# Kernel optimization log

Hardware: AMD Instinct MI355X
Metric: run time of the kernel (lower is better)

The kernel has to match this reference:

```python
import jax, jax.numpy as jnp
import numpy as np


def setup_inputs() -> dict:
    key = jax.random.key(0)
    k1, k2 = jax.random.split(key)
    B, H, W, C = 32, 32, 32, 256
    N_EMBED = 1024
    z = jax.random.normal(k1, (B, H, W, C), dtype=jnp.float32)
    emb_weights = jax.random.normal(k2, (N_EMBED, C), dtype=jnp.float32)
    return {"z": z, "emb_weights": emb_weights}


def reference(z, emb_weights):
    # z: (B,H,W,C) -> flatten to (N, C)
    B = z.shape[0]
    C = z.shape[-1]
    z_flat = z.reshape(-1, C)  # (N, C)
    # Squared euclidean distance via ||z||^2 + ||e||^2 - 2 z.e^T
    distance = (
        jnp.sum(z_flat ** 2, axis=1, keepdims=True)          # (N, 1)
        + jnp.sum(emb_weights ** 2, axis=1)                   # (n_embed,)
        - 2.0 * jnp.dot(z_flat, emb_weights.T)                # (N, n_embed)
    )
    min_encoding_indices = jnp.argmin(distance, axis=1)       # (N,)
    z_q = emb_weights[min_encoding_indices].reshape(z.shape)  # (B,H,W,C)
    min_encoding_indices = min_encoding_indices.reshape(B, -1)
    return z_q, min_encoding_indices
```

## Files before the change

kernel.cpp:

```cpp
#include <hip/hip_runtime.h>

#define C_DIM 256
#define NCODE 1024
#define MARGIN1 0.35f
#define MARGIN2 0.02f

typedef __bf16 bf16x8 __attribute__((ext_vector_type(8)));
typedef float f32x4 __attribute__((ext_vector_type(4)));

#define WS_ENORM  0
#define WS_META   4096
#define WS_RLIST  8192
#define WS_RLIST2 139264
#define WS_BP     270336
#define WS_PB     1318912
#define WS_PBI    2367488

#define BP_LO_OFF 262144

#define GLOAD_LDS16(g, s)                                                            \
  __builtin_amdgcn_global_load_lds(                                                  \
      (const __attribute__((address_space(1))) unsigned int*)(g),                    \
      (__attribute__((address_space(3))) unsigned int*)(s), 16, 0, 0)

__device__ __forceinline__ unsigned short bf16rne(float x) {
    unsigned u = __float_as_uint(x);
    return (unsigned short)((u + 0x7FFFu + ((u >> 16) & 1u)) >> 16);
}
__device__ __forceinline__ void bf16split(float x, unsigned short& h, unsigned short& l) {
    unsigned u  = __float_as_uint(x);
    unsigned rh = (u + 0x7FFFu + ((u >> 16) & 1u)) & 0xFFFF0000u;
    float    lf = x - __uint_as_float(rh);
    h = (unsigned short)(rh >> 16);
    l = bf16rne(lf);
}

__global__ __launch_bounds__(256) void prep_kernel(const float* __restrict__ emb,
                                                   unsigned short* __restrict__ bp,
                                                   float* __restrict__ enorm,
                                                   unsigned* __restrict__ meta) {
    int tid = blockIdx.x * 256 + threadIdx.x;
    if (tid < 2) meta[tid] = 0u;
    int j   = tid >> 5;
    int u   = tid & 31;
    int kc  = u >> 2, lg = u & 3;
    const float* src = emb + (size_t)j * C_DIM + kc * 32 + lg * 8;
    float4 v0 = *reinterpret_cast<const float4*>(src);
    float4 v1 = *reinterpret_cast<const float4*>(src + 4);
    float vs[8] = {v0.x, v0.y, v0.z, v0.w, v1.x, v1.y, v1.z, v1.w};
    unsigned short h[8], l[8];
    float s = 0.f;
    #pragma unroll
    for (int k = 0; k < 8; ++k) {
        bf16split(vs[k], h[k], l[k]);
        s = fmaf(vs[k], vs[k], s);
    }
    #pragma unroll
    for (int off = 1; off < 32; off <<= 1) s += __shfl_xor(s, off, 64);
    if (u == 0) enorm[j] = s;

    int chunk = j >> 5, nf = (j >> 4) & 1, lr = j & 15;
    int lane  = lg * 16 + lr;
    size_t base = (size_t)chunk * 8192 + (size_t)(nf * 8 + kc) * 512 + lane * 8;
    uint4 hp, lp;
    hp.x = (unsigned)h[0] | ((unsigned)h[1] << 16);
    hp.y = (unsigned)h[2] | ((unsigned)h[3] << 16);
    hp.z = (unsigned)h[4] | ((unsigned)h[5] << 16);
    hp.w = (unsigned)h[6] | ((unsigned)h[7] << 16);
    lp.x = (unsigned)l[0] | ((unsigned)l[1] << 16);
    lp.y = (unsigned)l[2] | ((unsigned)l[3] << 16);
    lp.z = (unsigned)l[4] | ((unsigned)l[5] << 16);
    lp.w = (unsigned)l[6] | ((unsigned)l[7] << 16);
    *reinterpret_cast<uint4*>(bp + base)             = hp;
    *reinterpret_cast<uint4*>(bp + BP_LO_OFF + base) = lp;
}

__global__ __launch_bounds__(256, 4) void vq_stage1_kernel(
    const float* __restrict__ z, const unsigned short* __restrict__ bp,
    const float* __restrict__ enorm, float2* __restrict__ pb,
    unsigned* __restrict__ pbi) {
    __shared__ unsigned short Bds[2][8192];
    __shared__ float en_s[256];

    const int t = threadIdx.x;
    const int w = t >> 6, lane = t & 63;
    const int lr = lane & 15, lg = lane >> 4;
    const int nq = blockIdx.x & 3;
    const long r0 = (long)(blockIdx.x >> 2) * 128 + w * 32;
    const unsigned short* bsrc = bp + (size_t)(nq * 8) * 8192 + lane * 8;

    en_s[t] = enorm[nq * 256 + t];

    bf16x8 ah[2][8];
    #pragma unroll
    for (int m = 0; m < 2; ++m) {
        const float* zr = z + (r0 + m * 16 + lr) * C_DIM + lg * 8;
        #pragma unroll
        for (int kc = 0; kc < 8; ++kc) {
            float4 v0 = *reinterpret_cast<const float4*>(zr + kc * 32);
            float4 v1 = *reinterpret_cast<const float4*>(zr + kc * 32 + 4);
            float vs[8] = {v0.x, v0.y, v0.z, v0.w, v1.x, v1.y, v1.z, v1.w};
            unsigned hp[4];
            #pragma unroll
            for (int p = 0; p < 4; ++p)
                hp[p] = (unsigned)bf16rne(vs[2 * p]) |
                        ((unsigned)bf16rne(vs[2 * p + 1]) << 16);
            ah[m][kc] = __builtin_bit_cast(bf16x8, *reinterpret_cast<uint4*>(hp));
        }
    }
    __syncthreads();

#define STG1(c, sl) {                                                   \
    unsigned short* db = &Bds[sl][0];                                   \
    const unsigned short* gs = bsrc + (size_t)(c) * 8192;               \
    _Pragma("unroll") for (int rd = 0; rd < 4; ++rd) {                  \
        int s_ = rd * 4 + w;                                            \
        GLOAD_LDS16(gs + s_ * 512, db + s_ * 512); } }

    STG1(0, 0);

    float b1[2][4], b2[2][4]; unsigned i1[2][4];
    #pragma unroll
    for (int m = 0; m < 2; ++m)
        #pragma unroll
        for (int r = 0; r < 4; ++r) { b1[m][r] = 3.4e38f; b2[m][r] = 3.4e38f; i1[m][r] = 0; }

    #pragma unroll 1
    for (int c = 0; c < 8; ++c) {
        asm volatile("s_waitcnt vmcnt(0)" ::: "memory");
        __builtin_amdgcn_s_barrier();
        if (c < 7) STG1(c + 1, (c + 1) & 1);

        f32x4 a00 = {0.f,0.f,0.f,0.f}, a01 = {0.f,0.f,0.f,0.f};
        f32x4 a10 = {0.f,0.f,0.f,0.f}, a11 = {0.f,0.f,0.f,0.f};
        const unsigned short* bb = &Bds[c & 1][lane * 8];
        __builtin_amdgcn_s_setprio(1);
        #pragma unroll
        for (int kc = 0; kc < 8; ++kc) {
            bf16x8 bh0 = *reinterpret_cast<const bf16x8*>(bb + kc * 512);
            bf16x8 bh1 = *reinterpret_cast<const bf16x8*>(bb + (8 + kc) * 512);
            a00 = __builtin_amdgcn_mfma_f32_16x16x32_bf16(ah[0][kc], bh0, a00, 0, 0, 0);
            a10 = __builtin_amdgcn_mfma_f32_16x16x32_bf16(ah[1][kc], bh0, a10, 0, 0, 0);
            a01 = __builtin_amdgcn_mfma_f32_16x16x32_bf16(ah[0][kc], bh1, a01, 0, 0, 0);
            a11 = __builtin_amdgcn_mfma_f32_16x16x32_bf16(ah[1][kc], bh1, a11, 0, 0, 0);
        }
        __builtin_amdgcn_s_setprio(0);

        #pragma unroll
        for (int nf = 0; nf < 2; ++nf) {
            const int cl = c * 32 + nf * 16 + lr;
            const float en = en_s[cl];
            const unsigned code = (unsigned)(nq * 256 + cl);
            #pragma unroll
            for (int r = 0; r < 4; ++r) {
                float d0 = fmaf(-2.f, (nf ? a01[r] : a00[r]), en);
                if (d0 < b1[0][r]) { b2[0][r] = b1[0][r]; b1[0][r] = d0; i1[0][r] = code; }
                else if (d0 < b2[0][r]) { b2[0][r] = d0; }
                float d1 = fmaf(-2.f, (nf ? a11[r] : a10[r]), en);
                if (d1 < b1[1][r]) { b2[1][r] = b1[1][r]; b1[1][r] = d1; i1[1][r] = code; }
                else if (d1 < b2[1][r]) { b2[1][r] = d1; }
            }
        }
    }
#undef STG1

    #pragma unroll
    for (int m = 0; m < 2; ++m)
        #pragma unroll
        for (int r = 0; r < 4; ++r) {
            float v1 = b1[m][r], v2 = b2[m][r]; unsigned j1 = i1[m][r];
            #pragma unroll
            for (int off = 8; off; off >>= 1) {
                float    ov1 = __shfl_xor(v1, off, 64);
                float    ov2 = __shfl_xor(v2, off, 64);
                unsigned oj1 = (unsigned)__shfl_xor((int)j1, off, 64);
                if (ov1 < v1 || (ov1 == v1 && oj1 < j1)) {
                    v2 = fminf(v1, ov2); v1 = ov1; j1 = oj1;
                } else {
                    v2 = fminf(v2, ov1);
                }
            }
            if (lr == 0) {
                long row = r0 + m * 16 + lg * 4 + r;
                pb [row * 4 + nq] = make_float2(v1, v2);
                pbi[row * 4 + nq] = j1;
            }
        }
}

__global__ __launch_bounds__(256) void finalize_gather_kernel(
    const float* __restrict__ emb, const float2* __restrict__ pb,
    const unsigned* __restrict__ pbi, float* __restrict__ zq,
    float* __restrict__ idx_out, unsigned* __restrict__ meta,
    unsigned* __restrict__ rlist, int n4) {
    const int lane = threadIdx.x & 63;
    for (long r4 = blockIdx.x; r4 < n4; r4 += gridDim.x) {
        const long row = r4 * 4 + (threadIdx.x >> 6);
        float B1 = 3.4e38f, B2 = 3.4e38f; unsigned I1 = 0;
        #pragma unroll
        for (int s = 0; s < 4; ++s) {
            float2   p = pb [row * 4 + s];
            unsigned j = pbi[row * 4 + s];
            if (p.x < B1) { B2 = fminf(B1, p.y); B1 = p.x; I1 = j; }
            else          { B2 = fminf(B2, p.x); }
        }
        if (lane == 0) {
            idx_out[row] = (float)I1;
            if (B2 - B1 <= MARGIN1) rlist[atomicAdd(meta, 1u)] = (unsigned)row;
        }
        float4 v = reinterpret_cast<const float4*>(emb)[(size_t)I1 * 64 + lane];
        reinterpret_cast<float4*>(zq)[row * 64 + lane] = v;
    }
}

__global__ __launch_bounds__(256) void vq_stage2_kernel(
    const float* __restrict__ z, const unsigned short* __restrict__ bp,
    const float* __restrict__ enorm, const float* __restrict__ emb,
    const unsigned* __restrict__ meta, const unsigned* __restrict__ rlist,
    float* __restrict__ zq, float* __restrict__ idx_out,
    unsigned* __restrict__ meta2, unsigned* __restrict__ rlist2) {
    __shared__ float en_s[NCODE];
    __shared__ float m1s[16][4], m2s[16][4];
    __shared__ unsigned mis[16][4];
    __shared__ unsigned codes_s[16];
    const int t = threadIdx.x, q = t >> 6, lane = t & 63;
    const int lr = lane & 15, lg = lane >> 4;
    en_s[t] = enorm[t]; en_s[t + 256] = enorm[t + 256];
    en_s[t + 512] = enorm[t + 512]; en_s[t + 768] = enorm[t + 768];
    __syncthreads();
    const unsigned cnt = meta[0];
    const unsigned ngroups = (cnt + 15) >> 4;

    for (unsigned g = blockIdx.x; g < ngroups; g += gridDim.x) {
        const unsigned base = g * 16;
        unsigned slot = base + (unsigned)lr;
        unsigned row = rlist[slot < cnt ? slot : 0];

        bf16x8 ah[8], al[8];
        const float* zr = z + (size_t)row * C_DIM + lg * 8;
        #pragma unroll
        for (int kc = 0; kc < 8; ++kc) {
            float4 v0 = *reinterpret_cast<const float4*>(zr + kc * 32);
            float4 v1 = *reinterpret_cast<const float4*>(zr + kc * 32 + 4);
            float vs[8] = {v0.x, v0.y, v0.z, v0.w, v1.x, v1.y, v1.z, v1.w};
            unsigned short hv[8], lv[8];
            #pragma unroll
            for (int jj = 0; jj < 8; ++jj) bf16split(vs[jj], hv[jj], lv[jj]);
            unsigned hp[4] = {
                (unsigned)hv[0] | ((unsigned)hv[1] << 16), (unsigned)hv[2] | ((unsigned)hv[3] << 16),
                (unsigned)hv[4] | ((unsigned)hv[5] << 16), (unsigned)hv[6] | ((unsigned)hv[7] << 16)};
            unsigned lp[4] = {
                (unsigned)lv[0] | ((unsigned)lv[1] << 16), (unsigned)lv[2] | ((unsigned)lv[3] << 16),
                (unsigned)lv[4] | ((unsigned)lv[5] << 16), (unsigned)lv[6] | ((unsigned)lv[7] << 16)};
            ah[kc] = __builtin_bit_cast(bf16x8, *reinterpret_cast<uint4*>(hp));
            al[kc] = __builtin_bit_cast(bf16x8, *reinterpret_cast<uint4*>(lp));
        }

        float b1[4], b2[4]; unsigned i1[4];
        #pragma unroll
        for (int r = 0; r < 4; ++r) { b1[r] = 3.4e38f; b2[r] = 3.4e38f; i1[r] = 0; }

        #pragma unroll 1
        for (int cc = 0; cc < 8; ++cc) {
            const int c = q * 8 + cc;
            f32x4 hh0 = {0.f,0.f,0.f,0.f}, hh1 = {0.f,0.f,0.f,0.f};
            f32x4 hl0 = {0.f,0.f,0.f,0.f}, hl1 = {0.f,0.f,0.f,0.f};
            f32x4 lh0 = {0.f,0.f,0.f,0.f}, lh1 = {0.f,0.f,0.f,0.f};
            const unsigned short* cb = bp + (size_t)c * 8192 + lane * 8;
            #pragma unroll
            for (int kc = 0; kc < 8; ++kc) {
                bf16x8 bh0 = *reinterpret_cast<const bf16x8*>(cb + kc * 512);
                bf16x8 bh1 = *reinterpret_cast<const bf16x8*>(cb + (8 + kc) * 512);
                bf16x8 bl0 = *reinterpret_cast<const bf16x8*>(cb + BP_LO_OFF + kc * 512);
                bf16x8 bl1 = *reinterpret_cast<const bf16x8*>(cb + BP_LO_OFF + (8 + kc) * 512);
                hh0 = __builtin_amdgcn_mfma_f32_16x16x32_bf16(ah[kc], bh0, hh0, 0, 0, 0);
                hh1 = __builtin_amdgcn_mfma_f32_16x16x32_bf16(ah[kc], bh1, hh1, 0, 0, 0);
                lh0 = __builtin_amdgcn_mfma_f32_16x16x32_bf16(al[kc], bh0, lh0, 0, 0, 0);
                lh1 = __builtin_amdgcn_mfma_f32_16x16x32_bf16(al[kc], bh1, lh1, 0, 0, 0);
                hl0 = __builtin_amdgcn_mfma_f32_16x16x32_bf16(ah[kc], bl0, hl0, 0, 0, 0);
                hl1 = __builtin_amdgcn_mfma_f32_16x16x32_bf16(ah[kc], bl1, hl1, 0, 0, 0);
            }
            #pragma unroll
            for (int nf = 0; nf < 2; ++nf) {
                const unsigned code = (unsigned)(c * 32 + nf * 16 + lr);
                const float en = en_s[code];
                #pragma unroll
                for (int r = 0; r < 4; ++r) {
                    float s3 = nf ? (hh1[r] + hl1[r] + lh1[r]) : (hh0[r] + hl0[r] + lh0[r]);
                    float d = fmaf(-2.f, s3, en);
                    if (d < b1[r]) { b2[r] = b1[r]; b1[r] = d; i1[r] = code; }
                    else if (d < b2[r]) { b2[r] = d; }
                }
            }
        }

        #pragma unroll
        for (int r = 0; r < 4; ++r) {
            float v1 = b1[r], v2 = b2[r]; unsigned j1 = i1[r];
            #pragma unroll
            for (int off = 8; off; off >>= 1) {
                float    ov1 = __shfl_xor(v1, off, 64);
                float    ov2 = __shfl_xor(v2, off, 64);
                unsigned oj1 = (unsigned)__shfl_xor((int)j1, off, 64);
                if (ov1 < v1 || (ov1 == v1 && oj1 < j1)) {
                    v2 = fminf(v1, ov2); v1 = ov1; j1 = oj1;
                } else {
                    v2 = fminf(v2, ov1);
                }
            }
            if (lr == 0) {
                int rg = lg * 4 + r;
                m1s[rg][q] = v1; m2s[rg][q] = v2; mis[rg][q] = j1;
            }
        }
        __syncthreads();
        if (t < 16) {
            float B1 = 3.4e38f, B2 = 3.4e38f; unsigned I1 = 0;
            #pragma unroll
            for (int s = 0; s < 4; ++s) {
                float v1 = m1s[t][s], v2 = m2s[t][s]; unsigned j = mis[t][s];
                if (v1 < B1) { B2 = fminf(B1, v2); B1 = v1; I1 = j; }
                else         { B2 = fminf(B2, v1); }
            }
            unsigned sl = base + (unsigned)t;
            codes_s[t] = I1;
            if (sl < cnt) {
                unsigned rrow = rlist[sl];
                idx_out[rrow] = (float)I1;
                if (B2 - B1 <= MARGIN2) rlist2[atomicAdd(meta2, 1u)] = rrow;
            }
        }
        __syncthreads();
        {
            int rr = t >> 4, seg = t & 15;
            unsigned sl = base + (unsigned)rr;
            if (sl < cnt) {
                unsigned rrow = rlist[sl];
                unsigned code = codes_s[rr];
                const float4* ep = reinterpret_cast<const float4*>(emb) + (size_t)code * 64 + seg * 4;
                float4*       op = reinterpret_cast<float4*>(zq) + (size_t)rrow * 64 + seg * 4;
                op[0] = ep[0]; op[1] = ep[1]; op[2] = ep[2]; op[3] = ep[3];
            }
        }
        __syncthreads();
    }
}

__global__ __launch_bounds__(256) void rescue_kernel(
    const float* __restrict__ z, const float* __restrict__ emb,
    const float* __restrict__ enorm, const unsigned* __restrict__ meta2,
    const unsigned* __restrict__ rlist2, float* __restrict__ zq,
    float* __restrict__ idx_out) {
    __shared__ float zrow[C_DIM];
    __shared__ float rd[256];
    __shared__ unsigned rix[256];
    const unsigned cnt = meta2[0];
    for (unsigned li = blockIdx.x; li < cnt; li += gridDim.x) {
        unsigned row = rlist2[li];
        __syncthreads();
        if (threadIdx.x < 64) {
            float4 v = reinterpret_cast<const float4*>(z)[(size_t)row * 64 + threadIdx.x];
            reinterpret_cast<float4*>(zrow)[threadIdx.x] = v;
        }
        __syncthreads();
        const int c = threadIdx.x;
        float a0 = 0.f, a1 = 0.f, a2 = 0.f, a3 = 0.f;
        const float4* zp = reinterpret_cast<const float4*>(zrow);
        const float4* e0 = reinterpret_cast<const float4*>(emb + (size_t)(c)       * C_DIM);
        const float4* e1 = reinterpret_cast<const float4*>(emb + (size_t)(c + 256) * C_DIM);
        const float4* e2 = reinterpret_cast<const float4*>(emb + (size_t)(c + 512) * C_DIM);
        const float4* e3 = reinterpret_cast<const float4*>(emb + (size_t)(c + 768) * C_DIM);
        #pragma unroll 8
        for (int k = 0; k < 64; ++k) {
            float4 z4 = zp[k];
            float4 f0 = e0[k], f1 = e1[k], f2 = e2[k], f3 = e3[k];
            a0 = fmaf(z4.x, f0.x, a0); a0 = fmaf(z4.y, f0.y, a0);
            a0 = fmaf(z4.z, f0.z, a0); a0 = fmaf(z4.w, f0.w, a0);
            a1 = fmaf(z4.x, f1.x, a1); a1 = fmaf(z4.y, f1.y, a1);
            a1 = fmaf(z4.z, f1.z, a1); a1 = fmaf(z4.w, f1.w, a1);
            a2 = fmaf(z4.x, f2.x, a2); a2 = fmaf(z4.y, f2.y, a2);
            a2 = fmaf(z4.z, f2.z, a2); a2 = fmaf(z4.w, f2.w, a2);
            a3 = fmaf(z4.x, f3.x, a3); a3 = fmaf(z4.y, f3.y, a3);
            a3 = fmaf(z4.z, f3.z, a3); a3 = fmaf(z4.w, f3.w, a3);
        }
        float d0 = fmaf(-2.f, a0, enorm[c]);
        float d1 = fmaf(-2.f, a1, enorm[c + 256]);
        float d2 = fmaf(-2.f, a2, enorm[c + 512]);
        float d3 = fmaf(-2.f, a3, enorm[c + 768]);
        float bd = d0; unsigned bi = (unsigned)c;
        if (d1 < bd) { bd = d1; bi = (unsigned)(c + 256); }
        if (d2 < bd) { bd = d2; bi = (unsigned)(c + 512); }
        if (d3 < bd) { bd = d3; bi = (unsigned)(c + 768); }
        rd[threadIdx.x] = bd; rix[threadIdx.x] = bi;
        __syncthreads();
        for (int s = 128; s; s >>= 1) {
            if (threadIdx.x < (unsigned)s) {
                float od = rd[threadIdx.x + s]; unsigned oi = rix[threadIdx.x + s];
                if (od < rd[threadIdx.x] ||
                    (od == rd[threadIdx.x] && oi < rix[threadIdx.x])) {
                    rd[threadIdx.x] = od; rix[threadIdx.x] = oi;
                }
            }
            __syncthreads();
        }
        unsigned code = rix[0];
        if (threadIdx.x < 64) {
            float4 v = reinterpret_cast<const float4*>(emb)[(size_t)code * 64 + threadIdx.x];
            reinterpret_cast<float4*>(zq)[(size_t)row * 64 + threadIdx.x] = v;
        }
        if (threadIdx.x == 0) idx_out[row] = (float)code;
    }
}

extern "C" void kernel_launch(void* const* d_in, const int* in_sizes, int n_in,
                              void* d_out, int out_size, void* d_ws, size_t ws_size,
                              hipStream_t stream) {
    const float* z   = (const float*)d_in[0];
    const float* emb = (const float*)d_in[1];
    const int n = in_sizes[0] / C_DIM;

    float* zq      = (float*)d_out;
    float* idx_out = zq + (size_t)n * C_DIM;

    char* ws = (char*)d_ws;
    float*          enorm  = (float*)(ws + WS_ENORM);
    unsigned*       meta   = (unsigned*)(ws + WS_META);
    unsigned*       rlist  = (unsigned*)(ws + WS_RLIST);
    unsigned*       rlist2 = (unsigned*)(ws + WS_RLIST2);
    unsigned short* bp     = (unsigned short*)(ws + WS_BP);
    float2*         pb     = (float2*)(ws + WS_PB);
    unsigned*       pbi    = (unsigned*)(ws + WS_PBI);

    prep_kernel<<<128, 256, 0, stream>>>(emb, bp, enorm, meta);
    vq_stage1_kernel<<<(n / 128) * 4, 256, 0, stream>>>(z, bp, enorm, pb, pbi);
    finalize_gather_kernel<<<2048, 256, 0, stream>>>(emb, pb, pbi, zq, idx_out,
                                                     meta, rlist, n / 4);
    vq_stage2_kernel<<<256, 256, 0, stream>>>(z, bp, enorm, emb, meta, rlist,
                                              zq, idx_out, meta + 1, rlist2);
    rescue_kernel<<<256, 256, 0, stream>>>(z, emb, enorm, meta + 1, rlist2,
                                           zq, idx_out);
}
```

Measured before the change: 135.5 us.

## Fuse finalize, stage-2 refinement and rescue into one per-block kernel

Replaces the finalize/gather, stage-2 refinement and rescue kernels with a single kernel in which each block handles 32 rows. Ambiguous rows are tracked in shared-memory lists rather than global atomic lists. This removes two kernel launches, the global atomic counters and the meta zeroing. In exchange, refinement and rescue work is no longer spread across blocks, so a block with many flagged rows serialises that work. The rescue loop runs fp32 matmuls inside a 256-thread block per row, which can create load imbalance.

```diff
diff --git a/kernel.cpp b/kernel.cpp
--- a/kernel.cpp
+++ b/kernel.cpp
@@ -9,13 +9,9 @@
 typedef float f32x4 __attribute__((ext_vector_type(4)));
 
 #define WS_ENORM  0
-#define WS_META   4096
-#define WS_RLIST  8192
-#define WS_RLIST2 139264
 #define WS_BP     270336
 #define WS_PB     1318912
 #define WS_PBI    2367488
-
 #define BP_LO_OFF 262144
 
 #define GLOAD_LDS16(g, s)                                                            \
@@ -37,10 +33,8 @@
 
 __global__ __launch_bounds__(256) void prep_kernel(const float* __restrict__ emb,
                                                    unsigned short* __restrict__ bp,
-                                                   float* __restrict__ enorm,
-                                                   unsigned* __restrict__ meta) {
+                                                   float* __restrict__ enorm) {
     int tid = blockIdx.x * 256 + threadIdx.x;
-    if (tid < 2) meta[tid] = 0u;
     int j   = tid >> 5;
     int u   = tid & 31;
     int kc  = u >> 2, lg = u & 3;
@@ -188,14 +182,35 @@
         }
 }
 
-__global__ __launch_bounds__(256) void finalize_gather_kernel(
-    const float* __restrict__ emb, const float2* __restrict__ pb,
-    const unsigned* __restrict__ pbi, float* __restrict__ zq,
-    float* __restrict__ idx_out, unsigned* __restrict__ meta,
-    unsigned* __restrict__ rlist, int n4) {
-    const int lane = threadIdx.x & 63;
-    for (long r4 = blockIdx.x; r4 < n4; r4 += gridDim.x) {
-        const long row = r4 * 4 + (threadIdx.x >> 6);
+__global__ __launch_bounds__(256) void finalize_all_kernel(
+    const float* __restrict__ z, const unsigned short* __restrict__ bp,
+    const float* __restrict__ enorm, const float* __restrict__ emb,
+    const float2* __restrict__ pb, const unsigned* __restrict__ pbi,
+    float* __restrict__ zq, float* __restrict__ idx_out) {
+    __shared__ float en_s[NCODE];
+    __shared__ float m1s[16][4], m2s[16][4];
+    __shared__ unsigned mis[16][4];
+    __shared__ unsigned codes_b[16];
+    __shared__ unsigned codes_a[32];
+    __shared__ unsigned flag_r[32];
+    __shared__ unsigned flag_n;
+    __shared__ unsigned resc_r[16];
+    __shared__ unsigned resc_n;
+    __shared__ float zrow[C_DIM];
+    __shared__ float rd[256];
+    __shared__ unsigned rix[256];
+
+    const int t = threadIdx.x, q = t >> 6, lane = t & 63;
+    const int lr = lane & 15, lg = lane >> 4;
+    const long r0 = (long)blockIdx.x * 32;
+
+    en_s[t] = enorm[t]; en_s[t + 256] = enorm[t + 256];
+    en_s[t + 512] = enorm[t + 512]; en_s[t + 768] = enorm[t + 768];
+    if (t == 0) flag_n = 0u;
+    __syncthreads();
+
+    if (t < 32) {
+        long row = r0 + t;
         float B1 = 3.4e38f, B2 = 3.4e38f; unsigned I1 = 0;
         #pragma unroll
         for (int s = 0; s < 4; ++s) {
@@ -204,37 +219,26 @@
             if (p.x < B1) { B2 = fminf(B1, p.y); B1 = p.x; I1 = j; }
             else          { B2 = fminf(B2, p.x); }
         }
-        if (lane == 0) {
-            idx_out[row] = (float)I1;
-            if (B2 - B1 <= MARGIN1) rlist[atomicAdd(meta, 1u)] = (unsigned)row;
-        }
-        float4 v = reinterpret_cast<const float4*>(emb)[(size_t)I1 * 64 + lane];
-        reinterpret_cast<float4*>(zq)[row * 64 + lane] = v;
-    }
-}
-
-__global__ __launch_bounds__(256) void vq_stage2_kernel(
-    const float* __restrict__ z, const unsigned short* __restrict__ bp,
-    const float* __restrict__ enorm, const float* __restrict__ emb,
-    const unsigned* __restrict__ meta, const unsigned* __restrict__ rlist,
-    float* __restrict__ zq, float* __restrict__ idx_out,
-    unsigned* __restrict__ meta2, unsigned* __restrict__ rlist2) {
-    __shared__ float en_s[NCODE];
-    __shared__ float m1s[16][4], m2s[16][4];
-    __shared__ unsigned mis[16][4];
-    __shared__ unsigned codes_s[16];
-    const int t = threadIdx.x, q = t >> 6, lane = t & 63;
-    const int lr = lane & 15, lg = lane >> 4;
-    en_s[t] = enorm[t]; en_s[t + 256] = enorm[t + 256];
-    en_s[t + 512] = enorm[t + 512]; en_s[t + 768] = enorm[t + 768];
+        idx_out[row] = (float)I1;
+        codes_a[t]   = I1;
+        if (B2 - B1 <= MARGIN1) flag_r[atomicAdd(&flag_n, 1u)] = (unsigned)row;
+    }
     __syncthreads();
-    const unsigned cnt = meta[0];
-    const unsigned ngroups = (cnt + 15) >> 4;
-
-    for (unsigned g = blockIdx.x; g < ngroups; g += gridDim.x) {
-        const unsigned base = g * 16;
+    {
+        int rr = t >> 3, seg = t & 7;
+        unsigned code = codes_a[rr];
+        const float4* ep = reinterpret_cast<const float4*>(emb) + (size_t)code * 64 + seg * 8;
+        float4*       op = reinterpret_cast<float4*>(zq) + ((size_t)(r0 + rr)) * 64 + seg * 8;
+        #pragma unroll
+        for (int j = 0; j < 8; ++j) op[j] = ep[j];
+    }
+    __syncthreads();
+
+    const unsigned nflag = flag_n;
+    for (unsigned base = 0; base < nflag; base += 16) {
         unsigned slot = base + (unsigned)lr;
-        unsigned row = rlist[slot < cnt ? slot : 0];
+        unsigned row = flag_r[slot < nflag ? slot : 0];
+        if (t == 0) resc_n = 0u;
 
         bf16x8 ah[8], al[8];
         const float* zr = z + (size_t)row * C_DIM + lg * 8;
@@ -323,92 +327,83 @@
                 else         { B2 = fminf(B2, v1); }
             }
             unsigned sl = base + (unsigned)t;
-            codes_s[t] = I1;
-            if (sl < cnt) {
-                unsigned rrow = rlist[sl];
+            codes_b[t] = I1;
+            if (sl < nflag) {
+                unsigned rrow = flag_r[sl];
                 idx_out[rrow] = (float)I1;
-                if (B2 - B1 <= MARGIN2) rlist2[atomicAdd(meta2, 1u)] = rrow;
+                if (B2 - B1 <= MARGIN2) resc_r[atomicAdd(&resc_n, 1u)] = rrow;
             }
         }
         __syncthreads();
         {
             int rr = t >> 4, seg = t & 15;
             unsigned sl = base + (unsigned)rr;
-            if (sl < cnt) {
-                unsigned rrow = rlist[sl];
-                unsigned code = codes_s[rr];
+            if (sl < nflag) {
+                unsigned rrow = flag_r[sl];
+                unsigned code = codes_b[rr];
                 const float4* ep = reinterpret_cast<const float4*>(emb) + (size_t)code * 64 + seg * 4;
                 float4*       op = reinterpret_cast<float4*>(zq) + (size_t)rrow * 64 + seg * 4;
                 op[0] = ep[0]; op[1] = ep[1]; op[2] = ep[2]; op[3] = ep[3];
             }
         }
         __syncthreads();
-    }
-}
-
-__global__ __launch_bounds__(256) void rescue_kernel(
-    const float* __restrict__ z, const float* __restrict__ emb,
-    const float* __restrict__ enorm, const unsigned* __restrict__ meta2,
-    const unsigned* __restrict__ rlist2, float* __restrict__ zq,
-    float* __restrict__ idx_out) {
-    __shared__ float zrow[C_DIM];
-    __shared__ float rd[256];
-    __shared__ unsigned rix[256];
-    const unsigned cnt = meta2[0];
-    for (unsigned li = blockIdx.x; li < cnt; li += gridDim.x) {
-        unsigned row = rlist2[li];
+
+        const unsigned nresc = resc_n;
+        for (unsigned ri = 0; ri < nresc; ++ri) {
+            unsigned rrow = resc_r[ri];
+            if (t < 64) {
+                float4 v = reinterpret_cast<const float4*>(z)[(size_t)rrow * 64 + t];
+                reinterpret_cast<float4*>(zrow)[t] = v;
+            }
+            __syncthreads();
+            const int c = t;
+            float a0 = 0.f, a1 = 0.f, a2 = 0.f, a3 = 0.f;
+            const float4* zp = reinterpret_cast<const float4*>(zrow);
+            const float4* e0 = reinterpret_cast<const float4*>(emb + (size_t)(c)       * C_DIM);
+            const float4* e1 = reinterpret_cast<const float4*>(emb + (size_t)(c + 256) * C_DIM);
+            const float4* e2 = reinterpret_cast<const float4*>(emb + (size_t)(c + 512) * C_DIM);
+            const float4* e3 = reinterpret_cast<const float4*>(emb + (size_t)(c + 768) * C_DIM);
+            #pragma unroll 8
+            for (int k = 0; k < 64; ++k) {
+                float4 z4 = zp[k];
+                float4 f0 = e0[k], f1 = e1[k], f2 = e2[k], f3 = e3[k];
+                a0 = fmaf(z4.x, f0.x, a0); a0 = fmaf(z4.y, f0.y, a0);
+                a0 = fmaf(z4.z, f0.z, a0); a0 = fmaf(z4.w, f0.w, a0);
+                a1 = fmaf(z4.x, f1.x, a1); a1 = fmaf(z4.y, f1.y, a1);
+                a1 = fmaf(z4.z, f1.z, a1); a1 = fmaf(z4.w, f1.w, a1);
+                a2 = fmaf(z4.x, f2.x, a2); a2 = fmaf(z4.y, f2.y, a2);
+                a2 = fmaf(z4.z, f2.z, a2); a2 = fmaf(z4.w, f2.w, a2);
+                a3 = fmaf(z4.x, f3.x, a3); a3 = fmaf(z4.y, f3.y, a3);
+                a3 = fmaf(z4.z, f3.z, a3); a3 = fmaf(z4.w, f3.w, a3);
+            }
+            float d0 = fmaf(-2.f, a0, en_s[c]);
+            float d1 = fmaf(-2.f, a1, en_s[c + 256]);
+            float d2 = fmaf(-2.f, a2, en_s[c + 512]);
+            float d3 = fmaf(-2.f, a3, en_s[c + 768]);
+            float bd = d0; unsigned bi = (unsigned)c;
+            if (d1 < bd) { bd = d1; bi = (unsigned)(c + 256); }
+            if (d2 < bd) { bd = d2; bi = (unsigned)(c + 512); }
+            if (d3 < bd) { bd = d3; bi = (unsigned)(c + 768); }
+            rd[t] = bd; rix[t] = bi;
+            __syncthreads();
+            for (int s = 128; s; s >>= 1) {
+                if (t < s) {
+                    float od = rd[t + s]; unsigned oi = rix[t + s];
+                    if (od < rd[t] || (od == rd[t] && oi < rix[t])) {
+                        rd[t] = od; rix[t] = oi;
+                    }
+                }
+                __syncthreads();
+            }
+            unsigned code = rix[0];
+            if (t < 64) {
+                float4 v = reinterpret_cast<const float4*>(emb)[(size_t)code * 64 + t];
+                reinterpret_cast<float4*>(zq)[(size_t)rrow * 64 + t] = v;
+            }
+            if (t == 0) idx_out[rrow] = (float)code;
+            __syncthreads();
+        }
         __syncthreads();
-        if (threadIdx.x < 64) {
-            float4 v = reinterpret_cast<const float4*>(z)[(size_t)row * 64 + threadIdx.x];
-            reinterpret_cast<float4*>(zrow)[threadIdx.x] = v;
-        }
-        __syncthreads();
-        const int c = threadIdx.x;
-        float a0 = 0.f, a1 = 0.f, a2 = 0.f, a3 = 0.f;
-        const float4* zp = reinterpret_cast<const float4*>(zrow);
-        const float4* e0 = reinterpret_cast<const float4*>(emb + (size_t)(c)       * C_DIM);
-        const float4* e1 = reinterpret_cast<const float4*>(emb + (size_t)(c + 256) * C_DIM);
-        const float4* e2 = reinterpret_cast<const float4*>(emb + (size_t)(c + 512) * C_DIM);
-        const float4* e3 = reinterpret_cast<const float4*>(emb + (size_t)(c + 768) * C_DIM);
-        #pragma unroll 8
-        for (int k = 0; k < 64; ++k) {
-            float4 z4 = zp[k];
-            float4 f0 = e0[k], f1 = e1[k], f2 = e2[k], f3 = e3[k];
-            a0 = fmaf(z4.x, f0.x, a0); a0 = fmaf(z4.y, f0.y, a0);
-            a0 = fmaf(z4.z, f0.z, a0); a0 = fmaf(z4.w, f0.w, a0);
-            a1 = fmaf(z4.x, f1.x, a1); a1 = fmaf(z4.y, f1.y, a1);
-            a1 = fmaf(z4.z, f1.z, a1); a1 = fmaf(z4.w, f1.w, a1);
-            a2 = fmaf(z4.x, f2.x, a2); a2 = fmaf(z4.y, f2.y, a2);
-            a2 = fmaf(z4.z, f2.z, a2); a2 = fmaf(z4.w, f2.w, a2);
-            a3 = fmaf(z4.x, f3.x, a3); a3 = fmaf(z4.y, f3.y, a3);
-            a3 = fmaf(z4.z, f3.z, a3); a3 = fmaf(z4.w, f3.w, a3);
-        }
-        float d0 = fmaf(-2.f, a0, enorm[c]);
-        float d1 = fmaf(-2.f, a1, enorm[c + 256]);
-        float d2 = fmaf(-2.f, a2, enorm[c + 512]);
-        float d3 = fmaf(-2.f, a3, enorm[c + 768]);
-        float bd = d0; unsigned bi = (unsigned)c;
-        if (d1 < bd) { bd = d1; bi = (unsigned)(c + 256); }
-        if (d2 < bd) { bd = d2; bi = (unsigned)(c + 512); }
-        if (d3 < bd) { bd = d3; bi = (unsigned)(c + 768); }
-        rd[threadIdx.x] = bd; rix[threadIdx.x] = bi;
-        __syncthreads();
-        for (int s = 128; s; s >>= 1) {
-            if (threadIdx.x < (unsigned)s) {
-                float od = rd[threadIdx.x + s]; unsigned oi = rix[threadIdx.x + s];
-                if (od < rd[threadIdx.x] ||
-                    (od == rd[threadIdx.x] && oi < rix[threadIdx.x])) {
-                    rd[threadIdx.x] = od; rix[threadIdx.x] = oi;
-                }
-            }
-            __syncthreads();
-        }
-        unsigned code = rix[0];
-        if (threadIdx.x < 64) {
-            float4 v = reinterpret_cast<const float4*>(emb)[(size_t)code * 64 + threadIdx.x];
-            reinterpret_cast<float4*>(zq)[(size_t)row * 64 + threadIdx.x] = v;
-        }
-        if (threadIdx.x == 0) idx_out[row] = (float)code;
     }
 }
 
@@ -423,20 +418,13 @@
     float* idx_out = zq + (size_t)n * C_DIM;
 
     char* ws = (char*)d_ws;
-    float*          enorm  = (float*)(ws + WS_ENORM);
-    unsigned*       meta   = (unsigned*)(ws + WS_META);
-    unsigned*       rlist  = (unsigned*)(ws + WS_RLIST);
-    unsigned*       rlist2 = (unsigned*)(ws + WS_RLIST2);
-    unsigned short* bp     = (unsigned short*)(ws + WS_BP);
-    float2*         pb     = (float2*)(ws + WS_PB);
-    unsigned*       pbi    = (unsigned*)(ws + WS_PBI);
-
-    prep_kernel<<<128, 256, 0, stream>>>(emb, bp, enorm, meta);
+    float*          enorm = (float*)(ws + WS_ENORM);
+    unsigned short* bp    = (unsigned short*)(ws + WS_BP);
+    float2*         pb    = (float2*)(ws + WS_PB);
+    unsigned*       pbi   = (unsigned*)(ws + WS_PBI);
+
+    prep_kernel<<<128, 256, 0, stream>>>(emb, bp, enorm);
     vq_stage1_kernel<<<(n / 128) * 4, 256, 0, stream>>>(z, bp, enorm, pb, pbi);
-    finalize_gather_kernel<<<2048, 256, 0, stream>>>(emb, pb, pbi, zq, idx_out,
-                                                     meta, rlist, n / 4);
-    vq_stage2_kernel<<<256, 256, 0, stream>>>(z, bp, enorm, emb, meta, rlist,
-                                              zq, idx_out, meta + 1, rlist2);
-    rescue_kernel<<<256, 256, 0, stream>>>(z, emb, enorm, meta + 1, rlist2,
-                                           zq, idx_out);
-}
+    finalize_all_kernel<<<n / 32, 256, 0, stream>>>(z, bp, enorm, emb, pb, pbi,
+                                                    zq, idx_out);
+}
```

Measured after the change: 170.3 us. 25.7% more time.
